# Kernel tuning notes

Measured on AMD Instinct MI355X. Metric: run time of the kernel, lower is better.

Reference implementation:

```python
import jax, jax.numpy as jnp
import numpy as np

EPS = 1e-5  # torch LayerNorm default


def setup_inputs() -> dict:
    key = jax.random.key(0)
    ks = jax.random.split(key, 4)
    N, E, D_IN, D_OUT = 10000, 640000, 128, 128
    x = jax.random.normal(ks[0], (N, D_IN), dtype=jnp.float32)
    edge_index = jax.random.randint(ks[1], (2, E), 0, N, dtype=jnp.int64)
    edge_weight = jax.random.uniform(ks[2], (E,), dtype=jnp.float32)
    W = jax.random.normal(ks[3], (D_IN, D_OUT), dtype=jnp.float32) / np.sqrt(D_IN)
    b = jnp.zeros((D_OUT,), dtype=jnp.float32)
    gamma = jnp.ones((D_OUT,), dtype=jnp.float32)
    beta = jnp.zeros((D_OUT,), dtype=jnp.float32)
    return {"x": x, "edge_index": edge_index, "edge_weight": edge_weight,
            "W": W, "b": b, "gamma": gamma, "beta": beta}


def reference(x, edge_index, edge_weight, W, b, gamma, beta):
    N = x.shape[0]
    src, dst = edge_index[0], edge_index[1]
    # in-degree (scatter_add of ones onto dst)
    deg = jax.ops.segment_sum(jnp.ones(dst.shape[0], dtype=x.dtype), dst,
                              num_segments=N)
    deg_inv = (deg + 1.0) ** -0.5  # [N]
    # gather-scale: per-edge messages [E, D]
    msgs = x[src] * deg_inv[src][:, None] * edge_weight[:, None]
    # scatter-add aggregation back to nodes [N, D]
    agg = jax.ops.segment_sum(msgs, dst, num_segments=N)
    agg = agg * deg_inv[:, None] + x  # symmetric norm + residual
    # linear + exact gelu (torch default) ; dropout is identity at eval
    h = jax.nn.gelu(agg @ W + b, approximate=False)
    # LayerNorm over last dim
    mu = jnp.mean(h, axis=-1, keepdims=True)
    var = jnp.mean((h - mu) ** 2, axis=-1, keepdims=True)
    return (h - mu) * jax.lax.rsqrt(var + EPS) * gamma + beta
```

## Files before the change

kernel.cpp:

```cpp
#include <hip/hip_runtime.h>
#include <math.h>


#define D 128
#define NB 512
#define NBK 256
#define MAXCHUNK 2560
#define MAXB 1600
#define FPSCALE 2097152.0f
#define FPINV (1.0f / 2097152.0f)

typedef short bf16x8 __attribute__((ext_vector_type(8)));
typedef float f32x4 __attribute__((ext_vector_type(4)));

static __device__ __forceinline__ unsigned bf16bits(float v) {
    unsigned u = __float_as_uint(v);
    return (u + 0x7fffu + ((u >> 16) & 1u)) >> 16;
}
static __device__ __forceinline__ int bkt_of(int d, unsigned N) {
    return (int)(((unsigned)d * NB) / N);
}
static __device__ __forceinline__ int bkt_start(int b, unsigned N) {
    return (int)(((unsigned)b * N + NB - 1) / NB);
}

__global__ __launch_bounds__(1024) void k_scatter(const int* __restrict__ srcIdx,
                                                  const int* __restrict__ dstIdx,
                                                  const float* __restrict__ ew,
                                                  uint2* __restrict__ tmp,
                                                  int* __restrict__ rp,
                                                  int E, int chunk, unsigned N) {
    __shared__ int hist[NB];
    __shared__ int scn[NB];
    __shared__ int cur[NB];
    __shared__ int dsts[MAXCHUNK];
    __shared__ uint2 sbuf[MAXCHUNK];
    int t = threadIdx.x, bb = blockIdx.x;
    int e0 = bb * chunk;
    int e1 = e0 + chunk; if (e1 > E) e1 = E;
    int n_loc = e1 - e0; if (n_loc < 0) n_loc = 0;
    for (int i = t; i < NB; i += 1024) hist[i] = 0;
    __syncthreads();
    for (int i = t; i < n_loc; i += 1024) {
        int d = dstIdx[e0 + i];
        dsts[i] = d;
        atomicAdd(&hist[bkt_of(d, N)], 1);
    }
    __syncthreads();
    if (t < NB) scn[t] = hist[t];
    __syncthreads();
    for (int o = 1; o < NB; o <<= 1) {
        int v = 0;
        if (t < NB && t >= o) v = scn[t - o];
        __syncthreads();
        if (t < NB && t >= o) scn[t] += v;
        __syncthreads();
    }
    if (t < NB) {
        int excl = scn[t] - hist[t];
        cur[t] = excl;
        rp[bb * (NB + 1) + t] = excl;
    }
    if (t == 0) rp[bb * (NB + 1) + NB] = n_loc;
    __syncthreads();
    for (int i = t; i < n_loc; i += 1024) {
        int d = dsts[i];
        int bin = bkt_of(d, N);
        int dl = d - bkt_start(bin, N);
        int pos = atomicAdd(&cur[bin], 1);
        sbuf[pos] = make_uint2((unsigned)srcIdx[e0 + i] | ((unsigned)dl << 16),
                               __float_as_uint(ew[e0 + i]));
    }
    __syncthreads();
    for (int i = t; i < n_loc; i += 1024)
        tmp[e0 + i] = sbuf[i];
}

__global__ __launch_bounds__(256) void k_build(const float* __restrict__ x,
                                               const uint2* __restrict__ tmp,
                                               const int* __restrict__ rp,
                                               unsigned* __restrict__ fin_g,
                                               int* __restrict__ stg,
                                               unsigned* __restrict__ xs,
                                               int chunk, unsigned N) {
    __shared__ int segoff[NBK];
    __shared__ int segsrc[NBK];
    __shared__ uint2 buf[MAXB];
    __shared__ unsigned finL[MAXB];
    __shared__ int h[24], st[24], cur[24];
    __shared__ float dinv[24];
    int b = blockIdx.x, t = threadIdx.x;
    int start = bkt_start(b, N), end = bkt_start(b + 1, N);
    int nn = end - start;
    if (t < NBK) {
        int lo = rp[t * (NB + 1) + b];
        int hi = rp[t * (NB + 1) + b + 1];
        segoff[t] = hi - lo;
        segsrc[t] = t * chunk + lo;
    }
    if (t < 24) h[t] = 0;
    __syncthreads();
    for (int o = 1; o < NBK; o <<= 1) {
        int v = 0;
        if (t < NBK && t >= o) v = segoff[t - o];
        __syncthreads();
        if (t < NBK && t >= o) segoff[t] += v;
        __syncthreads();
    }
    int cnt = segoff[NBK - 1];
    int cntc = cnt > MAXB ? MAXB : cnt;
    for (int i = t; i < cntc; i += 256) {
        int lo2 = 0, hi2 = NBK - 1;
        while (lo2 < hi2) { int mid = (lo2 + hi2) >> 1; if (segoff[mid] > i) hi2 = mid; else lo2 = mid + 1; }
        int base = lo2 ? segoff[lo2 - 1] : 0;
        uint2 rec = tmp[segsrc[lo2] + (i - base)];
        buf[i] = rec;
        atomicAdd(&h[rec.x >> 16], 1);
    }
    __syncthreads();
    if (t == 0) {
        st[0] = 0;
        for (int d2 = 0; d2 < nn; ++d2) st[d2 + 1] = st[d2] + h[d2];
    }
    if (t < nn) dinv[t] = rsqrtf((float)h[t] + 1.0f);
    __syncthreads();
    if (t < nn) cur[t] = st[t];
    __syncthreads();
    for (int i = t; i < cntc; i += 256) {
        uint2 rec = buf[i];
        int dl = (int)(rec.x >> 16);
        int pos = atomicAdd(&cur[dl], 1);
        finL[pos] = (rec.x & 0xffffu) | (bf16bits(__uint_as_float(rec.y)) << 16);
    }
    __syncthreads();
    for (int i = t; i < cntc; i += 256)
        fin_g[b * MAXB + i] = finL[i];
    if (t <= nn) stg[b * 32 + t] = st[t];
    for (int i = t; i < nn * 64; i += 256) {
        int nl = i >> 6, l = i & 63;
        int node = start + nl;
        float s = dinv[nl];
        float f0 = x[node * D + l] * s;
        float f1 = x[node * D + 64 + l] * s;
        xs[node * 64 + l] = bf16bits(f0) | (bf16bits(f1) << 16);
    }
}

__global__ __launch_bounds__(512) void k_mega(
    const float* __restrict__ x, const unsigned* __restrict__ xs,
    const unsigned* __restrict__ fin_g, const int* __restrict__ stg,
    const float* __restrict__ W, const float* __restrict__ bias,
    const float* __restrict__ gamma, const float* __restrict__ beta,
    float* __restrict__ out, unsigned N) {
    __shared__ unsigned short wb[16384];
    __shared__ __align__(16) char regA[8704];
    __shared__ __align__(16) char regB[10320];
    __shared__ int st[24];
    __shared__ float bias_s[128], gamma_s[128], beta_s[128];
    __shared__ float s1s[4][2], s2s[4][2];

    unsigned* finL = (unsigned*)regA;
    unsigned short* absb = (unsigned short*)regA;
    int* acc = (int*)regB;
    float* hls = (float*)regB;

    int b = blockIdx.x, t = threadIdx.x;
    int start = bkt_start(b, N), end = bkt_start(b + 1, N);
    int nn = end - start;
    int wv = t >> 6, l = t & 63;

    for (int idx = t; idx < D * D; idx += 512) {
        int k = idx >> 7, n = idx & 127;
        wb[((k >> 3) * 128 + n) * 8 + (k & 7)] = (unsigned short)bf16bits(W[idx]);
    }
    if (t < 128) { bias_s[t] = bias[t]; gamma_s[t] = gamma[t]; beta_s[t] = beta[t]; }
    if (t <= nn) st[t] = stg[b * 32 + t];
    for (int i = t; i < 20 * 128; i += 512) acc[i] = 0;
    __syncthreads();
    int cntc = st[nn];
    for (int i = t; i < cntc; i += 512) finL[i] = fin_g[b * MAXB + i];
    __syncthreads();

    {
        int lo = (int)(((long long)cntc * wv) >> 3);
        int hi = (int)(((long long)cntc * (wv + 1)) >> 3);
        if (lo < hi) {
            int dl = 0;
            while (st[dl + 1] <= lo) ++dl;
            float a0 = 0.0f, a1 = 0.0f;
            int i = lo;
            while (i < hi) {
                if (i >= st[dl + 1]) {
                    atomicAdd(&acc[dl * 128 + l], (int)(a0 * FPSCALE));
                    atomicAdd(&acc[dl * 128 + 64 + l], (int)(a1 * FPSCALE));
                    a0 = 0.0f; a1 = 0.0f;
                    do { ++dl; } while (i >= st[dl + 1]);
                }
                int stop = st[dl + 1] < hi ? st[dl + 1] : hi;
                for (; i + 8 <= stop; i += 8) {
                    unsigned p[8], q[8];
#pragma unroll
                    for (int j = 0; j < 8; ++j) p[j] = finL[i + j];
#pragma unroll
                    for (int j = 0; j < 8; ++j) q[j] = xs[(p[j] & 0xffffu) * 64u + (unsigned)l];
#pragma unroll
                    for (int j = 0; j < 8; ++j) {
                        float wt = __uint_as_float(p[j] & 0xffff0000u);
                        a0 = fmaf(__uint_as_float(q[j] << 16), wt, a0);
                        a1 = fmaf(__uint_as_float(q[j] & 0xffff0000u), wt, a1);
                    }
                }
                for (; i < stop; ++i) {
                    unsigned p = finL[i];
                    float wt = __uint_as_float(p & 0xffff0000u);
                    unsigned q = xs[(p & 0xffffu) * 64u + (unsigned)l];
                    a0 = fmaf(__uint_as_float(q << 16), wt, a0);
                    a1 = fmaf(__uint_as_float(q & 0xffff0000u), wt, a1);
                }
            }
            atomicAdd(&acc[dl * 128 + l], (int)(a0 * FPSCALE));
            atomicAdd(&acc[dl * 128 + 64 + l], (int)(a1 * FPSCALE));
        }
    }
    __syncthreads();

    for (int i = t; i < 32 * 128; i += 512) {
        int row = i >> 7, col = i & 127;
        unsigned short v = 0;
        if (row < nn) {
            float dv = rsqrtf((float)(st[row + 1] - st[row]) + 1.0f);
            float aggv = (float)acc[row * 128 + col] * FPINV * dv
                         + x[(start + row) * D + col];
            v = (unsigned short)bf16bits(aggv);
        }
        absb[row * 136 + col] = v;
    }
    __syncthreads();

    {
        int col = l & 15, quad = l >> 4;
#pragma unroll
        for (int ti = 0; ti < 2; ++ti) {
            int tid = wv * 2 + ti;
            int mt = tid >> 3, nt = tid & 7;
            f32x4 dacc = {0.0f, 0.0f, 0.0f, 0.0f};
#pragma unroll
            for (int kk = 0; kk < 4; ++kk) {
                bf16x8 av = *(const bf16x8*)&absb[(mt * 16 + col) * 136 + kk * 32 + quad * 8];
                bf16x8 bv = *(const bf16x8*)&wb[((kk * 4 + quad) * 128 + nt * 16 + col) * 8];
                dacc = __builtin_amdgcn_mfma_f32_16x16x32_bf16(av, bv, dacc, 0, 0, 0);
            }
#pragma unroll
            for (int r = 0; r < 4; ++r) {
                int m = mt * 16 + quad * 4 + r;
                int n = nt * 16 + col;
                if (m < 20) {
                    float hh = dacc[r] + bias_s[n];
                    hh = 0.5f * hh * (1.0f + erff(hh * 0.70710678f));
                    hls[m * 129 + n] = hh;
                }
            }
        }
    }
    __syncthreads();

    {
        int g = t >> 7;
        int tt = t & 127;
        int w2 = (t >> 6) & 1;
        for (int r = 0; r < 5; ++r) {
            int dl = r * 4 + g;
            bool valid = dl < nn;
            float hh = valid ? hls[dl * 129 + tt] : 0.0f;
            float v1 = hh, v2 = hh * hh;
#pragma unroll
            for (int o = 32; o > 0; o >>= 1) {
                v1 += __shfl_xor(v1, o, 64);
                v2 += __shfl_xor(v2, o, 64);
            }
            if (l == 0) { s1s[g][w2] = v1; s2s[g][w2] = v2; }
            __syncthreads();
            float s1 = s1s[g][0] + s1s[g][1];
            float s2 = s2s[g][0] + s2s[g][1];
            float mu = s1 * (1.0f / D);
            float var = s2 * (1.0f / D) - mu * mu;
            float rinv = rsqrtf(var + 1e-5f);
            if (valid)
                out[(start + dl) * D + tt] = (hh - mu) * rinv * gamma_s[tt] + beta_s[tt];
            __syncthreads();
        }
    }
}

static inline size_t align256(size_t v) { return (v + 255) & ~(size_t)255; }

extern "C" void kernel_launch(void* const* d_in, const int* in_sizes, int n_in,
                              void* d_out, int out_size, void* d_ws, size_t ws_size,
                              hipStream_t stream) {
    const float* x     = (const float*)d_in[0];
    const int*   ei    = (const int*)d_in[1];
    const float* ew    = (const float*)d_in[2];
    const float* W     = (const float*)d_in[3];
    const float* b     = (const float*)d_in[4];
    const float* gamma = (const float*)d_in[5];
    const float* beta  = (const float*)d_in[6];
    float* out = (float*)d_out;

    const int E = in_sizes[2];
    const unsigned N = (unsigned)(in_sizes[0] / D);
    const int chunk = (E + NBK - 1) / NBK;
    const int* srcIdx = ei;
    const int* dstIdx = ei + E;

    char* ws = (char*)d_ws;
    size_t off = 0;
    uint2* tmp = (uint2*)(ws + off);        off += align256((size_t)E * 8);
    int* rp = (int*)(ws + off);             off += align256((size_t)NBK * (NB + 1) * 4);
    unsigned* xs = (unsigned*)(ws + off);   off += align256((size_t)N * 64 * 4);
    unsigned* fin_g = (unsigned*)(ws + off); off += align256((size_t)NB * MAXB * 4);
    int* stg = (int*)(ws + off);            off += align256((size_t)NB * 32 * 4);
    (void)ws_size; (void)n_in; (void)out_size;

    k_scatter<<<NBK, 1024, 0, stream>>>(srcIdx, dstIdx, ew, tmp, rp, E, chunk, N);
    k_build<<<NB, 256, 0, stream>>>(x, tmp, rp, fin_g, stg, xs, chunk, N);
    k_mega<<<NB, 512, 0, stream>>>(x, xs, fin_g, stg, W, b, gamma, beta, out, N);
}
```

Measured before the change: 114.8 us.

## Use wave-shuffle scans, precompute bf16 W once, and simplify LayerNorm epilogue

Replaces the barrier-heavy shared-memory Hillis-Steele scans in k_scatter and k_build with wave-level shuffle scans plus a small cross-wave prefix. W is converted to the bf16 MFMA layout once, by extra blocks in k_scatter, instead of in every k_mega block, and k_mega copies it with vector loads. k_build gathers each segment per thread instead of binary-searching per record. The LayerNorm epilogue now handles one row per wave without block barriers. k_scatter rereads dstIdx from global instead of caching it, and serial per-thread segment copies may be unbalanced.

```diff
diff --git a/kernel.cpp b/kernel.cpp
--- a/kernel.cpp
+++ b/kernel.cpp
@@ -5,7 +5,6 @@
 #define D 128
 #define NB 512
 #define NBK 256
-#define MAXCHUNK 2560
 #define MAXB 1600
 #define FPSCALE 2097152.0f
 #define FPINV (1.0f / 2097152.0f)
@@ -27,44 +26,60 @@
 __global__ __launch_bounds__(1024) void k_scatter(const int* __restrict__ srcIdx,
                                                   const int* __restrict__ dstIdx,
                                                   const float* __restrict__ ew,
+                                                  const float* __restrict__ W,
                                                   uint2* __restrict__ tmp,
                                                   int* __restrict__ rp,
+                                                  unsigned short* __restrict__ wb_g,
                                                   int E, int chunk, unsigned N) {
+    int t = threadIdx.x, bb = blockIdx.x;
+    if (bb >= NBK) {
+        int base = (bb - NBK) * 2048;
+        for (int i = t; i < 2048; i += 1024) {
+            int idx = base + i;
+            int k = idx >> 7, n = idx & 127;
+            wb_g[((k >> 3) * 128 + n) * 8 + (k & 7)] = (unsigned short)bf16bits(W[idx]);
+        }
+        return;
+    }
     __shared__ int hist[NB];
-    __shared__ int scn[NB];
     __shared__ int cur[NB];
-    __shared__ int dsts[MAXCHUNK];
-    __shared__ uint2 sbuf[MAXCHUNK];
-    int t = threadIdx.x, bb = blockIdx.x;
+    __shared__ uint2 sbuf[MAXB + 1024];
+    __shared__ int wsum[8], wpre[8];
     int e0 = bb * chunk;
     int e1 = e0 + chunk; if (e1 > E) e1 = E;
     int n_loc = e1 - e0; if (n_loc < 0) n_loc = 0;
-    for (int i = t; i < NB; i += 1024) hist[i] = 0;
+    int l = t & 63;
+    if (t < NB) hist[t] = 0;
+    __syncthreads();
+    for (int i = t; i < n_loc; i += 1024)
+        atomicAdd(&hist[bkt_of(dstIdx[e0 + i], N)], 1);
+    __syncthreads();
+    int v = 0, incl = 0;
+    if (t < NB) {
+        v = hist[t];
+        incl = v;
+        for (int o = 1; o < 64; o <<= 1) {
+            int nb2 = __shfl_up(incl, o, 64);
+            if (l >= o) incl += nb2;
+        }
+        if (l == 63) wsum[t >> 6] = incl;
+    }
+    __syncthreads();
+    if (t < 8) {
+        int p = 0;
+        for (int i = 0; i < t; ++i) p += wsum[i];
+        wpre[t] = p;
+    }
+    __syncthreads();
+    if (t < NB) {
+        int excl = incl - v + wpre[t >> 6];
+        cur[t] = excl;
+        rp[bb * (NB + 1) + t] = excl;
+    }
+    if (t == 0) rp[bb * (NB + 1) + NB] = n_loc;
     __syncthreads();
     for (int i = t; i < n_loc; i += 1024) {
         int d = dstIdx[e0 + i];
-        dsts[i] = d;
-        atomicAdd(&hist[bkt_of(d, N)], 1);
-    }
-    __syncthreads();
-    if (t < NB) scn[t] = hist[t];
-    __syncthreads();
-    for (int o = 1; o < NB; o <<= 1) {
-        int v = 0;
-        if (t < NB && t >= o) v = scn[t - o];
-        __syncthreads();
-        if (t < NB && t >= o) scn[t] += v;
-        __syncthreads();
-    }
-    if (t < NB) {
-        int excl = scn[t] - hist[t];
-        cur[t] = excl;
-        rp[bb * (NB + 1) + t] = excl;
-    }
-    if (t == 0) rp[bb * (NB + 1) + NB] = n_loc;
-    __syncthreads();
-    for (int i = t; i < n_loc; i += 1024) {
-        int d = dsts[i];
         int bin = bkt_of(d, N);
         int dl = d - bkt_start(bin, N);
         int pos = atomicAdd(&cur[bin], 1);
@@ -76,46 +91,57 @@
         tmp[e0 + i] = sbuf[i];
 }
 
-__global__ __launch_bounds__(256) void k_build(const float* __restrict__ x,
+__global__ __launch_bounds__(512) void k_build(const float* __restrict__ x,
                                                const uint2* __restrict__ tmp,
                                                const int* __restrict__ rp,
                                                unsigned* __restrict__ fin_g,
                                                int* __restrict__ stg,
                                                unsigned* __restrict__ xs,
                                                int chunk, unsigned N) {
-    __shared__ int segoff[NBK];
-    __shared__ int segsrc[NBK];
     __shared__ uint2 buf[MAXB];
     __shared__ unsigned finL[MAXB];
     __shared__ int h[24], st[24], cur[24];
     __shared__ float dinv[24];
+    __shared__ int wsum[4], wpre[4];
     int b = blockIdx.x, t = threadIdx.x;
     int start = bkt_start(b, N), end = bkt_start(b + 1, N);
     int nn = end - start;
+    int l = t & 63;
+    int seglen = 0, segsrc = 0;
     if (t < NBK) {
         int lo = rp[t * (NB + 1) + b];
         int hi = rp[t * (NB + 1) + b + 1];
-        segoff[t] = hi - lo;
-        segsrc[t] = t * chunk + lo;
+        seglen = hi - lo;
+        segsrc = t * chunk + lo;
     }
     if (t < 24) h[t] = 0;
-    __syncthreads();
-    for (int o = 1; o < NBK; o <<= 1) {
-        int v = 0;
-        if (t < NBK && t >= o) v = segoff[t - o];
-        __syncthreads();
-        if (t < NBK && t >= o) segoff[t] += v;
-        __syncthreads();
-    }
-    int cnt = segoff[NBK - 1];
+    int incl = seglen;
+    if (t < NBK) {
+        for (int o = 1; o < 64; o <<= 1) {
+            int nb2 = __shfl_up(incl, o, 64);
+            if (l >= o) incl += nb2;
+        }
+        if (l == 63) wsum[t >> 6] = incl;
+    }
+    __syncthreads();
+    if (t < 4) {
+        int p = 0;
+        for (int i = 0; i < t; ++i) p += wsum[i];
+        wpre[t] = p;
+    }
+    __syncthreads();
+    int cnt = wsum[0] + wsum[1] + wsum[2] + wsum[3];
     int cntc = cnt > MAXB ? MAXB : cnt;
-    for (int i = t; i < cntc; i += 256) {
-        int lo2 = 0, hi2 = NBK - 1;
-        while (lo2 < hi2) { int mid = (lo2 + hi2) >> 1; if (segoff[mid] > i) hi2 = mid; else lo2 = mid + 1; }
-        int base = lo2 ? segoff[lo2 - 1] : 0;
-        uint2 rec = tmp[segsrc[lo2] + (i - base)];
-        buf[i] = rec;
-        atomicAdd(&h[rec.x >> 16], 1);
+    if (t < NBK && seglen > 0) {
+        int base = incl - seglen + wpre[t >> 6];
+        for (int k2 = 0; k2 < seglen; ++k2) {
+            int pos = base + k2;
+            if (pos < MAXB) {
+                uint2 rec = tmp[segsrc + k2];
+                buf[pos] = rec;
+                atomicAdd(&h[rec.x >> 16], 1);
+            }
+        }
     }
     __syncthreads();
     if (t == 0) {
@@ -126,38 +152,37 @@
     __syncthreads();
     if (t < nn) cur[t] = st[t];
     __syncthreads();
-    for (int i = t; i < cntc; i += 256) {
+    for (int i = t; i < cntc; i += 512) {
         uint2 rec = buf[i];
         int dl = (int)(rec.x >> 16);
         int pos = atomicAdd(&cur[dl], 1);
         finL[pos] = (rec.x & 0xffffu) | (bf16bits(__uint_as_float(rec.y)) << 16);
     }
     __syncthreads();
-    for (int i = t; i < cntc; i += 256)
+    for (int i = t; i < cntc; i += 512)
         fin_g[b * MAXB + i] = finL[i];
     if (t <= nn) stg[b * 32 + t] = st[t];
-    for (int i = t; i < nn * 64; i += 256) {
-        int nl = i >> 6, l = i & 63;
+    for (int i = t; i < nn * 64; i += 512) {
+        int nl = i >> 6, ll = i & 63;
         int node = start + nl;
         float s = dinv[nl];
-        float f0 = x[node * D + l] * s;
-        float f1 = x[node * D + 64 + l] * s;
-        xs[node * 64 + l] = bf16bits(f0) | (bf16bits(f1) << 16);
+        float f0 = x[node * D + ll] * s;
+        float f1 = x[node * D + 64 + ll] * s;
+        xs[node * 64 + ll] = bf16bits(f0) | (bf16bits(f1) << 16);
     }
 }
 
 __global__ __launch_bounds__(512) void k_mega(
     const float* __restrict__ x, const unsigned* __restrict__ xs,
     const unsigned* __restrict__ fin_g, const int* __restrict__ stg,
-    const float* __restrict__ W, const float* __restrict__ bias,
+    const unsigned short* __restrict__ wb_g, const float* __restrict__ bias,
     const float* __restrict__ gamma, const float* __restrict__ beta,
     float* __restrict__ out, unsigned N) {
-    __shared__ unsigned short wb[16384];
+    __shared__ __align__(16) unsigned short wb[16384];
     __shared__ __align__(16) char regA[8704];
     __shared__ __align__(16) char regB[10320];
     __shared__ int st[24];
     __shared__ float bias_s[128], gamma_s[128], beta_s[128];
-    __shared__ float s1s[4][2], s2s[4][2];
 
     unsigned* finL = (unsigned*)regA;
     unsigned short* absb = (unsigned short*)regA;
@@ -169,10 +194,8 @@
     int nn = end - start;
     int wv = t >> 6, l = t & 63;
 
-    for (int idx = t; idx < D * D; idx += 512) {
-        int k = idx >> 7, n = idx & 127;
-        wb[((k >> 3) * 128 + n) * 8 + (k & 7)] = (unsigned short)bf16bits(W[idx]);
-    }
+    for (int i = t; i < 2048; i += 512)
+        ((uint4*)wb)[i] = ((const uint4*)wb_g)[i];
     if (t < 128) { bias_s[t] = bias[t]; gamma_s[t] = gamma[t]; beta_s[t] = beta[t]; }
     if (t <= nn) st[t] = stg[b * 32 + t];
     for (int i = t; i < 20 * 128; i += 512) acc[i] = 0;
@@ -264,31 +287,22 @@
     }
     __syncthreads();
 
-    {
-        int g = t >> 7;
-        int tt = t & 127;
-        int w2 = (t >> 6) & 1;
-        for (int r = 0; r < 5; ++r) {
-            int dl = r * 4 + g;
-            bool valid = dl < nn;
-            float hh = valid ? hls[dl * 129 + tt] : 0.0f;
-            float v1 = hh, v2 = hh * hh;
-#pragma unroll
-            for (int o = 32; o > 0; o >>= 1) {
-                v1 += __shfl_xor(v1, o, 64);
-                v2 += __shfl_xor(v2, o, 64);
-            }
-            if (l == 0) { s1s[g][w2] = v1; s2s[g][w2] = v2; }
-            __syncthreads();
-            float s1 = s1s[g][0] + s1s[g][1];
-            float s2 = s2s[g][0] + s2s[g][1];
-            float mu = s1 * (1.0f / D);
-            float var = s2 * (1.0f / D) - mu * mu;
-            float rinv = rsqrtf(var + 1e-5f);
-            if (valid)
-                out[(start + dl) * D + tt] = (hh - mu) * rinv * gamma_s[tt] + beta_s[tt];
-            __syncthreads();
-        }
+    for (int r = wv; r < nn; r += 8) {
+        float h0 = hls[r * 129 + l];
+        float h1 = hls[r * 129 + 64 + l];
+        float v1 = h0 + h1;
+        float v2 = h0 * h0 + h1 * h1;
+#pragma unroll
+        for (int o = 32; o > 0; o >>= 1) {
+            v1 += __shfl_xor(v1, o, 64);
+            v2 += __shfl_xor(v2, o, 64);
+        }
+        float mu = v1 * (1.0f / D);
+        float var = v2 * (1.0f / D) - mu * mu;
+        float rinv = rsqrtf(var + 1e-5f);
+        int node = start + r;
+        out[node * D + l] = (h0 - mu) * rinv * gamma_s[l] + beta_s[l];
+        out[node * D + 64 + l] = (h1 - mu) * rinv * gamma_s[64 + l] + beta_s[64 + l];
     }
 }
 
@@ -314,14 +328,15 @@
 
     char* ws = (char*)d_ws;
     size_t off = 0;
-    uint2* tmp = (uint2*)(ws + off);        off += align256((size_t)E * 8);
-    int* rp = (int*)(ws + off);             off += align256((size_t)NBK * (NB + 1) * 4);
-    unsigned* xs = (unsigned*)(ws + off);   off += align256((size_t)N * 64 * 4);
+    uint2* tmp = (uint2*)(ws + off);         off += align256((size_t)E * 8);
+    int* rp = (int*)(ws + off);              off += align256((size_t)NBK * (NB + 1) * 4);
+    unsigned* xs = (unsigned*)(ws + off);    off += align256((size_t)N * 64 * 4);
     unsigned* fin_g = (unsigned*)(ws + off); off += align256((size_t)NB * MAXB * 4);
-    int* stg = (int*)(ws + off);            off += align256((size_t)NB * 32 * 4);
+    int* stg = (int*)(ws + off);             off += align256((size_t)NB * 32 * 4);
+    unsigned short* wb_g = (unsigned short*)(ws + off); off += align256((size_t)16384 * 2);
     (void)ws_size; (void)n_in; (void)out_size;
 
-    k_scatter<<<NBK, 1024, 0, stream>>>(srcIdx, dstIdx, ew, tmp, rp, E, chunk, N);
-    k_build<<<NB, 256, 0, stream>>>(x, tmp, rp, fin_g, stg, xs, chunk, N);
-    k_mega<<<NB, 512, 0, stream>>>(x, xs, fin_g, stg, W, b, gamma, beta, out, N);
-}
+    k_scatter<<<NBK + 8, 1024, 0, stream>>>(srcIdx, dstIdx, ew, W, tmp, rp, wb_g, E, chunk, N);
+    k_build<<<NB, 512, 0, stream>>>(x, tmp, rp, fin_g, stg, xs, chunk, N);
+    k_mega<<<NB, 512, 0, stream>>>(x, xs, fin_g, stg, wb_g, b, gamma, beta, out, N);
+}
```

Measured after the change: 112.0 us. -2.5%, faster.
